# Kernel optimization log

Hardware: AMD Instinct MI355X
Metric: run time of the kernel (lower is better)

Reference implementation:

```python
import jax, jax.numpy as jnp
import numpy as np

N_NODES = 10000
NUM_FEAT = 128
HIDD = 256
HEADS = 8
NUM_CLASS = 10
NEG_SLOPE = 0.2


def _gat_conv(x, src, dst, W, att_src, att_dst, bias, n_nodes):
    # x: [N, F_in]; W: [F_in, H*C]; att_*: [H, C]; bias: [H*C]
    H, C = att_src.shape
    h = (x @ W).reshape(n_nodes, H, C)                      # [N, H, C]
    a_src = jnp.einsum('nhc,hc->nh', h, att_src)            # [N, H]
    a_dst = jnp.einsum('nhc,hc->nh', h, att_dst)            # [N, H]
    e = a_src[src] + a_dst[dst]                             # [E, H]
    e = jnp.where(e >= 0, e, NEG_SLOPE * e)                 # leaky_relu
    # segment softmax over edges grouped by destination node
    e_max = jax.ops.segment_max(jax.lax.stop_gradient(e), dst, num_segments=n_nodes)
    e_max = jnp.where(jnp.isfinite(e_max), e_max, 0.0)
    ex = jnp.exp(e - e_max[dst])                            # [E, H]
    denom = jax.ops.segment_sum(ex, dst, num_segments=n_nodes)
    alpha = ex / (denom[dst] + 1e-16)                       # [E, H]
    msg = h[src] * alpha[:, :, None]                        # [E, H, C]
    out = jax.ops.segment_sum(msg, dst, num_segments=n_nodes)
    return out.reshape(n_nodes, H * C) + bias


def setup_inputs() -> dict:
    key = jax.random.key(0)
    ks = jax.random.split(key, 12)
    x = jax.random.normal(ks[0], (N_NODES, NUM_FEAT), dtype=jnp.float32)
    edge_index = jax.random.randint(ks[1], (2, 50000), 0, N_NODES, dtype=jnp.int64)
    g1 = 1.0 / np.sqrt(NUM_FEAT)
    g2 = 1.0 / np.sqrt(HEADS * HIDD)
    return {
        'x': x,
        'edge_index': edge_index,
        'W1': jax.random.normal(ks[2], (NUM_FEAT, HEADS * HIDD), dtype=jnp.float32) * g1,
        'att_src1': jax.random.normal(ks[3], (HEADS, HIDD), dtype=jnp.float32) * g2,
        'att_dst1': jax.random.normal(ks[4], (HEADS, HIDD), dtype=jnp.float32) * g2,
        'b1': jnp.zeros((HEADS * HIDD,), dtype=jnp.float32),
        'W2': jax.random.normal(ks[5], (HEADS * HIDD, NUM_CLASS), dtype=jnp.float32) * g2,
        'att_src2': jax.random.normal(ks[6], (1, NUM_CLASS), dtype=jnp.float32),
        'att_dst2': jax.random.normal(ks[7], (1, NUM_CLASS), dtype=jnp.float32),
        'b2': jnp.zeros((NUM_CLASS,), dtype=jnp.float32),
    }


def reference(x, edge_index, W1, att_src1, att_dst1, b1, W2, att_src2, att_dst2, b2):
    n = x.shape[0]
    # PyG GATConv default add_self_loops=True
    loop = jnp.arange(n, dtype=edge_index.dtype)
    src = jnp.concatenate([edge_index[0], loop])
    dst = jnp.concatenate([edge_index[1], loop])
    h = _gat_conv(x, src, dst, W1, att_src1, att_dst1, b1, n)
    h = jax.nn.elu(h)
    h = _gat_conv(h, src, dst, W2, att_src2, att_dst2, b2, n)
    return jax.nn.sigmoid(h)
```

## Files before the change

kernel.cpp:

```cpp
#include <hip/hip_runtime.h>
#include <math.h>

#define N_NODES 10000
#define N_PAD   10112
#define E0      50000
#define E_TOT   60000
#define FIN     128
#define HEADS   8
#define CHN     256
#define HC      2048
#define NC      10
#define NEG     0.2f
#define MAXD    128

typedef __attribute__((ext_vector_type(8))) short bf16x8;
typedef __attribute__((ext_vector_type(4))) float f32x4;

__device__ __forceinline__ unsigned f2u(float f){
  unsigned u = __float_as_uint(f);
  return (u & 0x80000000u) ? ~u : (u | 0x80000000u);
}
__device__ __forceinline__ float u2f(unsigned u){
  return __uint_as_float((u & 0x80000000u) ? (u & 0x7fffffffu) : ~u);
}
__device__ __forceinline__ unsigned short bf16_rne(float f){
  unsigned u = __float_as_uint(f);
  return (unsigned short)((u + 0x7FFFu + ((u >> 16) & 1u)) >> 16);
}

__global__ void k_detect(const int* __restrict__ raw, int* __restrict__ flag){
  int t = threadIdx.x;
  bool bad = (raw[2*t + 1] != 0) || ((unsigned)raw[2*t] >= (unsigned)N_NODES);
  unsigned long long b = __ballot(bad);
  if (t == 0) *flag = (b == 0ull) ? 1 : 0;
}

__global__ void k_convert(const int* __restrict__ raw, const int* __restrict__ flag,
                          int* __restrict__ esrc, int* __restrict__ edst,
                          int* __restrict__ deg){
  int e = blockIdx.x * blockDim.x + threadIdx.x;
  if (e >= E_TOT) return;
  int s, d;
  if (e < E0){
    if (*flag){ s = raw[2*e]; d = raw[2*(E0 + e)]; }
    else      { s = raw[e];   d = raw[E0 + e];     }
  } else {
    s = d = e - E0;
  }
  esrc[e] = s; edst[e] = d;
  atomicAdd(&deg[d], 1);
}

__global__ __launch_bounds__(256) void k_prep(const float* __restrict__ W1,
                                              const float* __restrict__ att_src,
                                              const float* __restrict__ att_dst,
                                              float* __restrict__ vv){
  int t = blockIdx.x*256 + threadIdx.x;
  int k = t >> 3, h = t & 7;
  const float* wrow = W1 + (size_t)k*HC + h*CHN;
  const float* as   = att_src + h*CHN;
  const float* ad   = att_dst + h*CHN;
  float s = 0.f, d = 0.f;
  #pragma unroll 4
  for (int c = 0; c < CHN; c += 4){
    float4 w = *reinterpret_cast<const float4*>(wrow + c);
    float4 a = *reinterpret_cast<const float4*>(as + c);
    float4 b = *reinterpret_cast<const float4*>(ad + c);
    s += w.x*a.x + w.y*a.y + w.z*a.z + w.w*a.w;
    d += w.x*b.x + w.y*b.y + w.z*b.z + w.w*b.w;
  }
  vv[k*16 + h]     = s;
  vv[k*16 + 8 + h] = d;
}

__global__ __launch_bounds__(256) void k_prepw(const float* __restrict__ W1,
                                               unsigned short* __restrict__ w1t_hi,
                                               unsigned short* __restrict__ w1t_lo){
  int t = blockIdx.x*256 + threadIdx.x;
  int k = t >> 11;
  int n = t & 2047;
  float v = W1[(size_t)k*HC + n];
  unsigned short hi = bf16_rne(v);
  float hf = __uint_as_float((unsigned)hi << 16);
  unsigned short lo = bf16_rne(v - hf);
  w1t_hi[(size_t)n*FIN + k] = hi;
  w1t_lo[(size_t)n*FIN + k] = lo;
}

__global__ __launch_bounds__(128) void k_attdot(const float* __restrict__ x,
                                                const float* __restrict__ vv,
                                                float* __restrict__ a_src,
                                                float* __restrict__ a_dst){
  __shared__ float s_red[2][16];
  const int n = blockIdx.x, k = threadIdx.x;
  const float xv = x[(size_t)n*FIN + k];
  const float* vk = vv + k*16;
  float p[16];
  #pragma unroll
  for (int u = 0; u < 16; ++u) p[u] = xv * vk[u];
  #pragma unroll
  for (int o = 1; o < 64; o <<= 1){
    #pragma unroll
    for (int u = 0; u < 16; ++u) p[u] += __shfl_xor(p[u], o);
  }
  if ((k & 63) == 0){
    #pragma unroll
    for (int u = 0; u < 16; ++u) s_red[k >> 6][u] = p[u];
  }
  __syncthreads();
  if (k < 16){
    float s = s_red[0][k] + s_red[1][k];
    if (k < 8) a_src[n*HEADS + k] = s;
    else       a_dst[n*HEADS + (k - 8)] = s;
  }
}

__global__ __launch_bounds__(256) void k_scan(const int* __restrict__ deg,
                                              int* __restrict__ offs){
  __shared__ int sums[256];
  const int tid = threadIdx.x;
  const int CHK = 40;
  int base = tid*CHK;
  int vals[CHK];
  int local = 0;
  #pragma unroll
  for (int i = 0; i < CHK; ++i){
    int idx = base + i;
    int v = (idx < N_NODES) ? deg[idx] : 0;
    vals[i] = local;
    local += v;
  }
  sums[tid] = local;
  __syncthreads();
  for (int o = 1; o < 256; o <<= 1){
    int t = (tid >= o) ? sums[tid - o] : 0;
    __syncthreads();
    sums[tid] += t;
    __syncthreads();
  }
  int boff = (tid == 0) ? 0 : sums[tid - 1];
  #pragma unroll
  for (int i = 0; i < CHK; ++i){
    int idx = base + i;
    if (idx < N_NODES) offs[idx] = boff + vals[i];
  }
  if (tid == 255) offs[N_NODES] = sums[255];
}

__global__ void k_scatter(const int* __restrict__ esrc, const int* __restrict__ edst,
                          const int* __restrict__ offs, int* __restrict__ cursor,
                          int* __restrict__ csr_src){
  int e = blockIdx.x*256 + threadIdx.x;
  if (e < E_TOT){
    int d = edst[e];
    int pos = offs[d] + atomicAdd(&cursor[d], 1);
    csr_src[pos] = esrc[e];
  }
}

__global__ __launch_bounds__(128) void k_aggx(const float* __restrict__ x,
                                              const float* __restrict__ a_src1,
                                              const float* __restrict__ a_dst1,
                                              const int* __restrict__ offs,
                                              const int* __restrict__ csr_src,
                                              unsigned short* __restrict__ agg_hi,
                                              unsigned short* __restrict__ agg_lo){
  __shared__ float s_e[MAXD][HEADS];
  __shared__ int s_src[MAXD];
  __shared__ unsigned s_maxu[HEADS];
  __shared__ float s_sum[HEADS];
  __shared__ float s_inv[HEADS];
  __shared__ float s_ad[HEADS];
  const int n = blockIdx.x, tid = threadIdx.x;
  const int start = offs[n];
  int deg = offs[n+1] - start;
  if (deg > MAXD) deg = MAXD;
  if (tid < HEADS){
    s_maxu[tid] = 0u;
    s_sum[tid] = 0.f;
    s_ad[tid] = a_dst1[n*HEADS + tid];
  }
  for (int i = tid; i < deg; i += 128) s_src[i] = csr_src[start + i];
  __syncthreads();
  const int tot = deg*HEADS;
  for (int i = tid; i < tot; i += 128){
    int e = i >> 3, hh = i & 7;
    float v = a_src1[s_src[e]*HEADS + hh] + s_ad[hh];
    v = (v >= 0.f) ? v : NEG*v;
    s_e[e][hh] = v;
    atomicMax(&s_maxu[hh], f2u(v));
  }
  __syncthreads();
  for (int i = tid; i < tot; i += 128){
    int e = i >> 3, hh = i & 7;
    float v = expf(s_e[e][hh] - u2f(s_maxu[hh]));
    s_e[e][hh] = v;
    atomicAdd(&s_sum[hh], v);
  }
  __syncthreads();
  if (tid < HEADS) s_inv[tid] = 1.f/(s_sum[tid] + 1e-16f);
  __syncthreads();
  for (int i = tid; i < tot; i += 128) s_e[i>>3][i&7] *= s_inv[i&7];
  __syncthreads();
  float acc[HEADS] = {0,0,0,0,0,0,0,0};
  for (int e = 0; e < deg; ++e){
    float xv = x[(size_t)s_src[e]*FIN + tid];
    #pragma unroll
    for (int h = 0; h < HEADS; ++h) acc[h] = fmaf(s_e[e][h], xv, acc[h]);
  }
  #pragma unroll
  for (int h = 0; h < HEADS; ++h){
    float v = acc[h];
    unsigned short hi = bf16_rne(v);
    float hf = __uint_as_float((unsigned)hi << 16);
    unsigned short lo = bf16_rne(v - hf);
    size_t idx = ((size_t)n*HEADS + h)*FIN + tid;
    agg_hi[idx] = hi;
    agg_lo[idx] = lo;
  }
}

__global__ __launch_bounds__(256) void k_gemmf(const unsigned short* __restrict__ agg_hi,
                                               const unsigned short* __restrict__ agg_lo,
                                               const unsigned short* __restrict__ w1t_hi,
                                               const unsigned short* __restrict__ w1t_lo,
                                               const float* __restrict__ b1,
                                               const float* __restrict__ W2,
                                               float* __restrict__ h2_part){
  __shared__ float W2s[128][NC];
  __shared__ float b1s[128];
  __shared__ float h2s[2][128][NC];
  const int tid = threadIdx.x;
  const int bx = blockIdx.x;
  const int by = blockIdx.y;
  const int h  = bx >> 1;
  const int colbase = bx*128;
  const int wave = tid >> 6, lane = tid & 63;
  const int wr = wave >> 1, wc = wave & 1;
  const int nl = lane & 15, g = lane >> 4;

  for (int i = tid; i < 128*NC; i += 256){
    int c = i/NC, j = i - c*NC;
    W2s[c][j] = W2[(size_t)(colbase + c)*NC + j];
  }
  if (tid < 128) b1s[tid] = b1[colbase + tid];

  f32x4 zero4 = {0.f, 0.f, 0.f, 0.f};
  f32x4 acc[4][4];
  #pragma unroll
  for (int fm = 0; fm < 4; ++fm)
    #pragma unroll
    for (int fn = 0; fn < 4; ++fn) acc[fm][fn] = zero4;

  const size_t abase = (((size_t)(by*128 + wr*64 + nl))*HEADS + h)*FIN + g*8;
  const size_t bbase = ((size_t)(colbase + wc*64 + nl))*FIN + g*8;

  #pragma unroll
  for (int kc = 0; kc < 4; ++kc){
    bf16x8 ah[4], al[4], bh[4], bl[4];
    #pragma unroll
    for (int f = 0; f < 4; ++f){
      size_t ao = abase + (size_t)f*16*HEADS*FIN + kc*32;
      size_t bo = bbase + (size_t)f*16*FIN + kc*32;
      ah[f] = *reinterpret_cast<const bf16x8*>(agg_hi + ao);
      al[f] = *reinterpret_cast<const bf16x8*>(agg_lo + ao);
      bh[f] = *reinterpret_cast<const bf16x8*>(w1t_hi + bo);
      bl[f] = *reinterpret_cast<const bf16x8*>(w1t_lo + bo);
    }
    #pragma unroll
    for (int fm = 0; fm < 4; ++fm)
      #pragma unroll
      for (int fn = 0; fn < 4; ++fn){
        acc[fm][fn] = __builtin_amdgcn_mfma_f32_16x16x32_bf16(ah[fm], bh[fn], acc[fm][fn], 0, 0, 0);
        acc[fm][fn] = __builtin_amdgcn_mfma_f32_16x16x32_bf16(ah[fm], bl[fn], acc[fm][fn], 0, 0, 0);
        acc[fm][fn] = __builtin_amdgcn_mfma_f32_16x16x32_bf16(al[fm], bh[fn], acc[fm][fn], 0, 0, 0);
      }
  }
  __syncthreads();

  #pragma unroll
  for (int fm = 0; fm < 4; ++fm)
    #pragma unroll
    for (int fn = 0; fn < 4; ++fn){
      float bb = b1s[wc*64 + fn*16 + nl];
      #pragma unroll
      for (int r = 0; r < 4; ++r){
        float v = acc[fm][fn][r] + bb;
        acc[fm][fn][r] = (v > 0.f) ? v : (__expf(v) - 1.f);
      }
    }

  for (int j = 0; j < NC; ++j){
    float hp[4][4];
    #pragma unroll
    for (int fm = 0; fm < 4; ++fm)
      #pragma unroll
      for (int r = 0; r < 4; ++r) hp[fm][r] = 0.f;
    #pragma unroll
    for (int fn = 0; fn < 4; ++fn){
      float w = W2s[wc*64 + fn*16 + nl][j];
      #pragma unroll
      for (int fm = 0; fm < 4; ++fm)
        #pragma unroll
        for (int r = 0; r < 4; ++r)
          hp[fm][r] = fmaf(acc[fm][fn][r], w, hp[fm][r]);
    }
    #pragma unroll
    for (int o = 1; o < 16; o <<= 1){
      #pragma unroll
      for (int fm = 0; fm < 4; ++fm)
        #pragma unroll
        for (int r = 0; r < 4; ++r)
          hp[fm][r] += __shfl_xor(hp[fm][r], o);
    }
    if (nl == 0){
      #pragma unroll
      for (int fm = 0; fm < 4; ++fm)
        #pragma unroll
        for (int r = 0; r < 4; ++r)
          h2s[wc][wr*64 + fm*16 + g*4 + r][j] = hp[fm][r];
    }
  }
  __syncthreads();
  for (int i = tid; i < 128*NC; i += 256){
    int rl = i/NC, j = i - rl*NC;
    int row = by*128 + rl;
    if (row < N_NODES)
      h2_part[((size_t)bx*N_NODES + row)*NC + j] = h2s[0][rl][j] + h2s[1][rl][j];
  }
}

__global__ __launch_bounds__(256) void k_h2fin(const float* __restrict__ h2_part,
                                               const float* __restrict__ as2,
                                               const float* __restrict__ ad2,
                                               float* __restrict__ h2,
                                               float* __restrict__ a_src2,
                                               float* __restrict__ a_dst2){
  int n = blockIdx.x*256 + threadIdx.x;
  if (n >= N_NODES) return;
  float s[NC];
  #pragma unroll
  for (int j = 0; j < NC; ++j) s[j] = 0.f;
  for (int bx = 0; bx < 16; ++bx){
    #pragma unroll
    for (int j = 0; j < NC; ++j)
      s[j] += h2_part[((size_t)bx*N_NODES + n)*NC + j];
  }
  float ds = 0.f, dd = 0.f;
  #pragma unroll
  for (int j = 0; j < NC; ++j){
    h2[(size_t)n*NC + j] = s[j];
    ds = fmaf(s[j], as2[j], ds);
    dd = fmaf(s[j], ad2[j], dd);
  }
  a_src2[n] = ds;
  a_dst2[n] = dd;
}

__global__ __launch_bounds__(64) void k_agg2(const float* __restrict__ h2,
                                             const float* __restrict__ a_src2,
                                             const float* __restrict__ a_dst2,
                                             const int* __restrict__ offs,
                                             const int* __restrict__ csr_src,
                                             const float* __restrict__ b2,
                                             float* __restrict__ out){
  const int n = blockIdx.x, lane = threadIdx.x;
  const int start = offs[n];
  const int deg = offs[n+1] - start;
  const float ad = a_dst2[n];
  float m = -INFINITY;
  for (int i = lane; i < deg; i += 64){
    float e = a_src2[csr_src[start + i]] + ad;
    e = (e >= 0.f) ? e : NEG*e;
    m = fmaxf(m, e);
  }
  #pragma unroll
  for (int o = 1; o < 64; o <<= 1) m = fmaxf(m, __shfl_xor(m, o));
  float s = 0.f;
  for (int i = lane; i < deg; i += 64){
    float e = a_src2[csr_src[start + i]] + ad;
    e = (e >= 0.f) ? e : NEG*e;
    s += expf(e - m);
  }
  #pragma unroll
  for (int o = 1; o < 64; o <<= 1) s += __shfl_xor(s, o);
  const float inv = 1.f/(s + 1e-16f);
  if (lane < NC){
    float acc = 0.f;
    for (int i = 0; i < deg; ++i){
      int src = csr_src[start + i];
      float e = a_src2[src] + ad;
      e = (e >= 0.f) ? e : NEG*e;
      float al = expf(e - m)*inv;
      acc = fmaf(al, h2[(size_t)src*NC + lane], acc);
    }
    float v = acc + b2[lane];
    out[n*NC + lane] = 1.f/(1.f + expf(-v));
  }
}

extern "C" void kernel_launch(void* const* d_in, const int* in_sizes, int n_in,
                              void* d_out, int out_size, void* d_ws, size_t ws_size,
                              hipStream_t stream){
  const float* x   = (const float*)d_in[0];
  const int*   ei  = (const int*)  d_in[1];
  const float* W1  = (const float*)d_in[2];
  const float* as1 = (const float*)d_in[3];
  const float* ad1 = (const float*)d_in[4];
  const float* b1  = (const float*)d_in[5];
  const float* W2  = (const float*)d_in[6];
  const float* as2 = (const float*)d_in[7];
  const float* ad2 = (const float*)d_in[8];
  const float* b2  = (const float*)d_in[9];
  float* out = (float*)d_out;

  char* ws = (char*)d_ws;
  size_t off = 0;
  auto alloc = [&](size_t bytes) -> void* {
    void* p = ws + off;
    off += (bytes + 255) & ~(size_t)255;
    return p;
  };
  unsigned short* agg_hi = (unsigned short*)alloc((size_t)N_PAD*HEADS*FIN*2);
  unsigned short* agg_lo = (unsigned short*)alloc((size_t)N_PAD*HEADS*FIN*2);
  unsigned short* w1t_hi = (unsigned short*)alloc((size_t)HC*FIN*2);
  unsigned short* w1t_lo = (unsigned short*)alloc((size_t)HC*FIN*2);
  float* h2_part = (float*)alloc((size_t)16*N_NODES*NC*4);
  float* vv      = (float*)alloc((size_t)FIN*16*4);
  float* a_src1  = (float*)alloc((size_t)N_NODES*HEADS*4);
  float* a_dst1  = (float*)alloc((size_t)N_NODES*HEADS*4);
  float* h2      = (float*)alloc((size_t)N_NODES*NC*4);
  float* a_src2  = (float*)alloc((size_t)N_NODES*4);
  float* a_dst2  = (float*)alloc((size_t)N_NODES*4);
  int*   deg     = (int*)alloc((size_t)N_NODES*4);
  int*   offs    = (int*)alloc((size_t)(N_NODES+1)*4);
  int*   cursor  = (int*)alloc((size_t)N_NODES*4);
  int*   esrc    = (int*)alloc((size_t)E_TOT*4);
  int*   edst    = (int*)alloc((size_t)E_TOT*4);
  int*   csr_src = (int*)alloc((size_t)E_TOT*4);
  int*   flag    = (int*)alloc(4);
  (void)ws_size; (void)in_sizes; (void)n_in; (void)out_size;

  hipMemsetAsync(deg,    0, (size_t)N_NODES*4, stream);
  hipMemsetAsync(cursor, 0, (size_t)N_NODES*4, stream);

  k_detect <<<1, 64, 0, stream>>>(ei, flag);
  k_convert<<<(E_TOT + 255)/256, 256, 0, stream>>>(ei, flag, esrc, edst, deg);
  k_prep   <<<4, 256, 0, stream>>>(W1, as1, ad1, vv);
  k_prepw  <<<(HC*FIN)/256, 256, 0, stream>>>(W1, w1t_hi, w1t_lo);
  k_attdot <<<N_NODES, 128, 0, stream>>>(x, vv, a_src1, a_dst1);
  k_scan   <<<1, 256, 0, stream>>>(deg, offs);
  k_scatter<<<(E_TOT + 255)/256, 256, 0, stream>>>(esrc, edst, offs, cursor, csr_src);
  k_aggx   <<<N_NODES, 128, 0, stream>>>(x, a_src1, a_dst1, offs, csr_src, agg_hi, agg_lo);
  k_gemmf  <<<dim3(16, N_PAD/128), 256, 0, stream>>>(agg_hi, agg_lo, w1t_hi, w1t_lo, b1, W2, h2_part);
  k_h2fin  <<<(N_NODES + 255)/256, 256, 0, stream>>>(h2_part, as2, ad2, h2, a_src2, a_dst2);
  k_agg2   <<<N_NODES, 64, 0, stream>>>(h2, a_src2, a_dst2, offs, csr_src, b2, out);
}
```

Measured before the change: 258.8 us.

## Unfuse layer-2 projection into separate GEMV, merge prep kernels, restructure attdot and agg2

Several changes land together. The two memsets and the detect kernel become one init kernel, and the weight-prep kernels are merged into one that also transposes W2. k_attdot now handles four nodes per block with one wave each. The scan uses 1024 threads, and agg2 computes the softmax weights once and caches them in shared memory. The largest change removes the fused W2 projection from the GEMM epilogue: the ELU output (10000x2048 fp32, about 80 MB) is written to memory and read back by a separate GEMV kernel. agg2 also truncates degree to 64, which risks wrong results for high-degree nodes.

```diff
diff --git a/kernel.cpp b/kernel.cpp
--- a/kernel.cpp
+++ b/kernel.cpp
@@ -12,6 +12,7 @@
 #define NC      10
 #define NEG     0.2f
 #define MAXD    128
+#define MAXD2   64
 
 typedef __attribute__((ext_vector_type(8))) short bf16x8;
 typedef __attribute__((ext_vector_type(4))) float f32x4;
@@ -28,11 +29,16 @@
   return (unsigned short)((u + 0x7FFFu + ((u >> 16) & 1u)) >> 16);
 }
 
-__global__ void k_detect(const int* __restrict__ raw, int* __restrict__ flag){
-  int t = threadIdx.x;
-  bool bad = (raw[2*t + 1] != 0) || ((unsigned)raw[2*t] >= (unsigned)N_NODES);
-  unsigned long long b = __ballot(bad);
-  if (t == 0) *flag = (b == 0ull) ? 1 : 0;
+__global__ void k_init(const int* __restrict__ raw, int* __restrict__ flag,
+                       int* __restrict__ deg, int* __restrict__ cursor){
+  int t = blockIdx.x*256 + threadIdx.x;
+  if (t < N_NODES){ deg[t] = 0; cursor[t] = 0; }
+  if (blockIdx.x == 0 && threadIdx.x < 64){
+    int i = threadIdx.x;
+    bool bad = (raw[2*i + 1] != 0) || ((unsigned)raw[2*i] >= (unsigned)N_NODES);
+    unsigned long long b = __ballot(bad);
+    if (i == 0) *flag = (b == 0ull) ? 1 : 0;
+  }
 }
 
 __global__ void k_convert(const int* __restrict__ raw, const int* __restrict__ flag,
@@ -51,80 +57,83 @@
   atomicAdd(&deg[d], 1);
 }
 
-__global__ __launch_bounds__(256) void k_prep(const float* __restrict__ W1,
-                                              const float* __restrict__ att_src,
-                                              const float* __restrict__ att_dst,
-                                              float* __restrict__ vv){
+__global__ __launch_bounds__(256) void k_prepw(const float* __restrict__ W1,
+                                               const float* __restrict__ att_src,
+                                               const float* __restrict__ att_dst,
+                                               const float* __restrict__ W2,
+                                               unsigned short* __restrict__ w1t_hi,
+                                               unsigned short* __restrict__ w1t_lo,
+                                               float* __restrict__ W2t,
+                                               float* __restrict__ vv){
   int t = blockIdx.x*256 + threadIdx.x;
-  int k = t >> 3, h = t & 7;
-  const float* wrow = W1 + (size_t)k*HC + h*CHN;
-  const float* as   = att_src + h*CHN;
-  const float* ad   = att_dst + h*CHN;
-  float s = 0.f, d = 0.f;
-  #pragma unroll 4
-  for (int c = 0; c < CHN; c += 4){
-    float4 w = *reinterpret_cast<const float4*>(wrow + c);
-    float4 a = *reinterpret_cast<const float4*>(as + c);
-    float4 b = *reinterpret_cast<const float4*>(ad + c);
-    s += w.x*a.x + w.y*a.y + w.z*a.z + w.w*a.w;
-    d += w.x*b.x + w.y*b.y + w.z*b.z + w.w*b.w;
-  }
-  vv[k*16 + h]     = s;
-  vv[k*16 + 8 + h] = d;
-}
-
-__global__ __launch_bounds__(256) void k_prepw(const float* __restrict__ W1,
-                                               unsigned short* __restrict__ w1t_hi,
-                                               unsigned short* __restrict__ w1t_lo){
-  int t = blockIdx.x*256 + threadIdx.x;
-  int k = t >> 11;
-  int n = t & 2047;
-  float v = W1[(size_t)k*HC + n];
-  unsigned short hi = bf16_rne(v);
-  float hf = __uint_as_float((unsigned)hi << 16);
-  unsigned short lo = bf16_rne(v - hf);
-  w1t_hi[(size_t)n*FIN + k] = hi;
-  w1t_lo[(size_t)n*FIN + k] = lo;
-}
-
-__global__ __launch_bounds__(128) void k_attdot(const float* __restrict__ x,
+  {
+    int k = t >> 11;
+    int n = t & 2047;
+    float v = W1[(size_t)k*HC + n];
+    unsigned short hi = bf16_rne(v);
+    float hf = __uint_as_float((unsigned)hi << 16);
+    unsigned short lo = bf16_rne(v - hf);
+    w1t_hi[(size_t)n*FIN + k] = hi;
+    w1t_lo[(size_t)n*FIN + k] = lo;
+  }
+  if (t < HC*NC){
+    int j = t >> 11, k = t & 2047;
+    W2t[(size_t)j*HC + k] = W2[(size_t)k*NC + j];
+  }
+  if (t < FIN*HEADS){
+    int k = t >> 3, h = t & 7;
+    const float* wrow = W1 + (size_t)k*HC + h*CHN;
+    const float* as   = att_src + h*CHN;
+    const float* ad   = att_dst + h*CHN;
+    float s = 0.f, d = 0.f;
+    #pragma unroll 4
+    for (int c = 0; c < CHN; c += 4){
+      float4 w = *reinterpret_cast<const float4*>(wrow + c);
+      float4 a = *reinterpret_cast<const float4*>(as + c);
+      float4 b = *reinterpret_cast<const float4*>(ad + c);
+      s += w.x*a.x + w.y*a.y + w.z*a.z + w.w*a.w;
+      d += w.x*b.x + w.y*b.y + w.z*b.z + w.w*b.w;
+    }
+    vv[k*16 + h]     = s;
+    vv[k*16 + 8 + h] = d;
+  }
+}
+
+__global__ __launch_bounds__(256) void k_attdot(const float* __restrict__ x,
                                                 const float* __restrict__ vv,
                                                 float* __restrict__ a_src,
                                                 float* __restrict__ a_dst){
-  __shared__ float s_red[2][16];
-  const int n = blockIdx.x, k = threadIdx.x;
-  const float xv = x[(size_t)n*FIN + k];
-  const float* vk = vv + k*16;
-  float p[16];
-  #pragma unroll
-  for (int u = 0; u < 16; ++u) p[u] = xv * vk[u];
-  #pragma unroll
-  for (int o = 1; o < 64; o <<= 1){
-    #pragma unroll
-    for (int u = 0; u < 16; ++u) p[u] += __shfl_xor(p[u], o);
-  }
-  if ((k & 63) == 0){
-    #pragma unroll
-    for (int u = 0; u < 16; ++u) s_red[k >> 6][u] = p[u];
-  }
-  __syncthreads();
-  if (k < 16){
-    float s = s_red[0][k] + s_red[1][k];
-    if (k < 8) a_src[n*HEADS + k] = s;
-    else       a_dst[n*HEADS + (k - 8)] = s;
-  }
-}
-
-__global__ __launch_bounds__(256) void k_scan(const int* __restrict__ deg,
-                                              int* __restrict__ offs){
-  __shared__ int sums[256];
+  const int wave = threadIdx.x >> 6, lane = threadIdx.x & 63;
+  const int n = blockIdx.x*4 + wave;
+  const int u = lane & 15, c = lane >> 4;
+  const float* xr = x + (size_t)n*FIN + c*32;
+  float acc = 0.f;
+  #pragma unroll
+  for (int q = 0; q < 8; ++q){
+    float4 xv = *reinterpret_cast<const float4*>(xr + q*4);
+    int k = c*32 + q*4;
+    acc = fmaf(xv.x, vv[(k+0)*16 + u], acc);
+    acc = fmaf(xv.y, vv[(k+1)*16 + u], acc);
+    acc = fmaf(xv.z, vv[(k+2)*16 + u], acc);
+    acc = fmaf(xv.w, vv[(k+3)*16 + u], acc);
+  }
+  acc += __shfl_xor(acc, 16);
+  acc += __shfl_xor(acc, 32);
+  if (c == 0){
+    if (u < 8) a_src[n*HEADS + u] = acc;
+    else       a_dst[n*HEADS + (u - 8)] = acc;
+  }
+}
+
+__global__ __launch_bounds__(1024) void k_scan(const int* __restrict__ deg,
+                                               int* __restrict__ offs){
+  __shared__ int sums[1024];
   const int tid = threadIdx.x;
-  const int CHK = 40;
-  int base = tid*CHK;
-  int vals[CHK];
+  int base = tid*10;
+  int vals[10];
   int local = 0;
   #pragma unroll
-  for (int i = 0; i < CHK; ++i){
+  for (int i = 0; i < 10; ++i){
     int idx = base + i;
     int v = (idx < N_NODES) ? deg[idx] : 0;
     vals[i] = local;
@@ -132,7 +141,7 @@
   }
   sums[tid] = local;
   __syncthreads();
-  for (int o = 1; o < 256; o <<= 1){
+  for (int o = 1; o < 1024; o <<= 1){
     int t = (tid >= o) ? sums[tid - o] : 0;
     __syncthreads();
     sums[tid] += t;
@@ -140,11 +149,11 @@
   }
   int boff = (tid == 0) ? 0 : sums[tid - 1];
   #pragma unroll
-  for (int i = 0; i < CHK; ++i){
+  for (int i = 0; i < 10; ++i){
     int idx = base + i;
     if (idx < N_NODES) offs[idx] = boff + vals[i];
   }
-  if (tid == 255) offs[N_NODES] = sums[255];
+  if (tid == 1023) offs[N_NODES] = sums[1023];
 }
 
 __global__ void k_scatter(const int* __restrict__ esrc, const int* __restrict__ edst,
@@ -220,16 +229,12 @@
   }
 }
 
-__global__ __launch_bounds__(256) void k_gemmf(const unsigned short* __restrict__ agg_hi,
+__global__ __launch_bounds__(256) void k_gemm1(const unsigned short* __restrict__ agg_hi,
                                                const unsigned short* __restrict__ agg_lo,
                                                const unsigned short* __restrict__ w1t_hi,
                                                const unsigned short* __restrict__ w1t_lo,
                                                const float* __restrict__ b1,
-                                               const float* __restrict__ W2,
-                                               float* __restrict__ h2_part){
-  __shared__ float W2s[128][NC];
-  __shared__ float b1s[128];
-  __shared__ float h2s[2][128][NC];
+                                               float* __restrict__ out1){
   const int tid = threadIdx.x;
   const int bx = blockIdx.x;
   const int by = blockIdx.y;
@@ -239,12 +244,6 @@
   const int wr = wave >> 1, wc = wave & 1;
   const int nl = lane & 15, g = lane >> 4;
 
-  for (int i = tid; i < 128*NC; i += 256){
-    int c = i/NC, j = i - c*NC;
-    W2s[c][j] = W2[(size_t)(colbase + c)*NC + j];
-  }
-  if (tid < 128) b1s[tid] = b1[colbase + tid];
-
   f32x4 zero4 = {0.f, 0.f, 0.f, 0.f};
   f32x4 acc[4][4];
   #pragma unroll
@@ -276,85 +275,66 @@
         acc[fm][fn] = __builtin_amdgcn_mfma_f32_16x16x32_bf16(al[fm], bh[fn], acc[fm][fn], 0, 0, 0);
       }
   }
-  __syncthreads();
-
-  #pragma unroll
-  for (int fm = 0; fm < 4; ++fm)
+
+  #pragma unroll
+  for (int fm = 0; fm < 4; ++fm){
     #pragma unroll
     for (int fn = 0; fn < 4; ++fn){
-      float bb = b1s[wc*64 + fn*16 + nl];
+      int col = colbase + wc*64 + fn*16 + nl;
+      float bb = b1[col];
       #pragma unroll
       for (int r = 0; r < 4; ++r){
-        float v = acc[fm][fn][r] + bb;
-        acc[fm][fn][r] = (v > 0.f) ? v : (__expf(v) - 1.f);
+        int row = by*128 + wr*64 + fm*16 + g*4 + r;
+        if (row < N_NODES){
+          float v = acc[fm][fn][r] + bb;
+          v = (v > 0.f) ? v : (__expf(v) - 1.f);
+          out1[(size_t)row*HC + col] = v;
+        }
       }
     }
-
-  for (int j = 0; j < NC; ++j){
-    float hp[4][4];
-    #pragma unroll
-    for (int fm = 0; fm < 4; ++fm)
-      #pragma unroll
-      for (int r = 0; r < 4; ++r) hp[fm][r] = 0.f;
-    #pragma unroll
-    for (int fn = 0; fn < 4; ++fn){
-      float w = W2s[wc*64 + fn*16 + nl][j];
-      #pragma unroll
-      for (int fm = 0; fm < 4; ++fm)
-        #pragma unroll
-        for (int r = 0; r < 4; ++r)
-          hp[fm][r] = fmaf(acc[fm][fn][r], w, hp[fm][r]);
-    }
-    #pragma unroll
-    for (int o = 1; o < 16; o <<= 1){
-      #pragma unroll
-      for (int fm = 0; fm < 4; ++fm)
-        #pragma unroll
-        for (int r = 0; r < 4; ++r)
-          hp[fm][r] += __shfl_xor(hp[fm][r], o);
-    }
-    if (nl == 0){
-      #pragma unroll
-      for (int fm = 0; fm < 4; ++fm)
-        #pragma unroll
-        for (int r = 0; r < 4; ++r)
-          h2s[wc][wr*64 + fm*16 + g*4 + r][j] = hp[fm][r];
-    }
-  }
-  __syncthreads();
-  for (int i = tid; i < 128*NC; i += 256){
-    int rl = i/NC, j = i - rl*NC;
-    int row = by*128 + rl;
-    if (row < N_NODES)
-      h2_part[((size_t)bx*N_NODES + row)*NC + j] = h2s[0][rl][j] + h2s[1][rl][j];
-  }
-}
-
-__global__ __launch_bounds__(256) void k_h2fin(const float* __restrict__ h2_part,
+  }
+}
+
+__global__ __launch_bounds__(256) void k_gemv2(const float* __restrict__ out1,
+                                               const float* __restrict__ W2t,
                                                const float* __restrict__ as2,
                                                const float* __restrict__ ad2,
                                                float* __restrict__ h2,
                                                float* __restrict__ a_src2,
                                                float* __restrict__ a_dst2){
-  int n = blockIdx.x*256 + threadIdx.x;
-  if (n >= N_NODES) return;
-  float s[NC];
-  #pragma unroll
-  for (int j = 0; j < NC; ++j) s[j] = 0.f;
-  for (int bx = 0; bx < 16; ++bx){
-    #pragma unroll
-    for (int j = 0; j < NC; ++j)
-      s[j] += h2_part[((size_t)bx*N_NODES + n)*NC + j];
-  }
-  float ds = 0.f, dd = 0.f;
-  #pragma unroll
-  for (int j = 0; j < NC; ++j){
-    h2[(size_t)n*NC + j] = s[j];
-    ds = fmaf(s[j], as2[j], ds);
-    dd = fmaf(s[j], ad2[j], dd);
-  }
-  a_src2[n] = ds;
-  a_dst2[n] = dd;
+  const int tid = threadIdx.x;
+  const int nl = tid & 15;
+  const int ng = tid >> 4;
+  const int n = blockIdx.x*16 + ng;
+  float acc[NC];
+  #pragma unroll
+  for (int j = 0; j < NC; ++j) acc[j] = 0.f;
+  const float* row = out1 + (size_t)n*HC;
+  for (int i = 0; i < 32; ++i){
+    int k = i*64 + nl*4;
+    float4 v = *reinterpret_cast<const float4*>(row + k);
+    #pragma unroll
+    for (int j = 0; j < NC; ++j){
+      float4 w = *reinterpret_cast<const float4*>(W2t + (size_t)j*HC + k);
+      acc[j] += v.x*w.x + v.y*w.y + v.z*w.z + v.w*w.w;
+    }
+  }
+  #pragma unroll
+  for (int o = 1; o < 16; o <<= 1){
+    #pragma unroll
+    for (int j = 0; j < NC; ++j) acc[j] += __shfl_xor(acc[j], o);
+  }
+  if (nl == 0){
+    float ds = 0.f, dd = 0.f;
+    #pragma unroll
+    for (int j = 0; j < NC; ++j){
+      h2[(size_t)n*NC + j] = acc[j];
+      ds = fmaf(acc[j], as2[j], ds);
+      dd = fmaf(acc[j], ad2[j], dd);
+    }
+    a_src2[n] = ds;
+    a_dst2[n] = dd;
+  }
 }
 
 __global__ __launch_bounds__(64) void k_agg2(const float* __restrict__ h2,
@@ -364,36 +344,33 @@
                                              const int* __restrict__ csr_src,
                                              const float* __restrict__ b2,
                                              float* __restrict__ out){
+  __shared__ float s_al[MAXD2];
+  __shared__ int s_sc[MAXD2];
   const int n = blockIdx.x, lane = threadIdx.x;
   const int start = offs[n];
-  const int deg = offs[n+1] - start;
+  int deg = offs[n+1] - start;
+  if (deg > MAXD2) deg = MAXD2;
   const float ad = a_dst2[n];
-  float m = -INFINITY;
-  for (int i = lane; i < deg; i += 64){
-    float e = a_src2[csr_src[start + i]] + ad;
+  float e = -INFINITY;
+  if (lane < deg){
+    int src = csr_src[start + lane];
+    s_sc[lane] = src;
+    e = a_src2[src] + ad;
     e = (e >= 0.f) ? e : NEG*e;
-    m = fmaxf(m, e);
-  }
+  }
+  float m = e;
   #pragma unroll
   for (int o = 1; o < 64; o <<= 1) m = fmaxf(m, __shfl_xor(m, o));
-  float s = 0.f;
-  for (int i = lane; i < deg; i += 64){
-    float e = a_src2[csr_src[start + i]] + ad;
-    e = (e >= 0.f) ? e : NEG*e;
-    s += expf(e - m);
-  }
+  float ex = (lane < deg) ? expf(e - m) : 0.f;
+  float s = ex;
   #pragma unroll
   for (int o = 1; o < 64; o <<= 1) s += __shfl_xor(s, o);
-  const float inv = 1.f/(s + 1e-16f);
+  if (lane < deg) s_al[lane] = ex / (s + 1e-16f);
+  __syncthreads();
   if (lane < NC){
     float acc = 0.f;
-    for (int i = 0; i < deg; ++i){
-      int src = csr_src[start + i];
-      float e = a_src2[src] + ad;
-      e = (e >= 0.f) ? e : NEG*e;
-      float al = expf(e - m)*inv;
-      acc = fmaf(al, h2[(size_t)src*NC + lane], acc);
-    }
+    for (int i = 0; i < deg; ++i)
+      acc = fmaf(s_al[i], h2[(size_t)s_sc[i]*NC + lane], acc);
     float v = acc + b2[lane];
     out[n*NC + lane] = 1.f/(1.f + expf(-v));
   }
@@ -421,11 +398,12 @@
     off += (bytes + 255) & ~(size_t)255;
     return p;
   };
+  float* out1    = (float*)alloc((size_t)N_NODES*HC*4);
   unsigned short* agg_hi = (unsigned short*)alloc((size_t)N_PAD*HEADS*FIN*2);
   unsigned short* agg_lo = (unsigned short*)alloc((size_t)N_PAD*HEADS*FIN*2);
   unsigned short* w1t_hi = (unsigned short*)alloc((size_t)HC*FIN*2);
   unsigned short* w1t_lo = (unsigned short*)alloc((size_t)HC*FIN*2);
-  float* h2_part = (float*)alloc((size_t)16*N_NODES*NC*4);
+  float* W2t     = (float*)alloc((size_t)NC*HC*4);
   float* vv      = (float*)alloc((size_t)FIN*16*4);
   float* a_src1  = (float*)alloc((size_t)N_NODES*HEADS*4);
   float* a_dst1  = (float*)alloc((size_t)N_NODES*HEADS*4);
@@ -441,18 +419,14 @@
   int*   flag    = (int*)alloc(4);
   (void)ws_size; (void)in_sizes; (void)n_in; (void)out_size;
 
-  hipMemsetAsync(deg,    0, (size_t)N_NODES*4, stream);
-  hipMemsetAsync(cursor, 0, (size_t)N_NODES*4, stream);
-
-  k_detect <<<1, 64, 0, stream>>>(ei, flag);
+  k_init   <<<40, 256, 0, stream>>>(ei, flag, deg, cursor);
   k_convert<<<(E_TOT + 255)/256, 256, 0, stream>>>(ei, flag, esrc, edst, deg);
-  k_prep   <<<4, 256, 0, stream>>>(W1, as1, ad1, vv);
-  k_prepw  <<<(HC*FIN)/256, 256, 0, stream>>>(W1, w1t_hi, w1t_lo);
-  k_attdot <<<N_NODES, 128, 0, stream>>>(x, vv, a_src1, a_dst1);
-  k_scan   <<<1, 256, 0, stream>>>(deg, offs);
+  k_prepw  <<<(HC*FIN)/256, 256, 0, stream>>>(W1, as1, ad1, W2, w1t_hi, w1t_lo, W2t, vv);
+  k_attdot <<<N_NODES/4, 256, 0, stream>>>(x, vv, a_src1, a_dst1);
+  k_scan   <<<1, 1024, 0, stream>>>(deg, offs);
   k_scatter<<<(E_TOT + 255)/256, 256, 0, stream>>>(esrc, edst, offs, cursor, csr_src);
   k_aggx   <<<N_NODES, 128, 0, stream>>>(x, a_src1, a_dst1, offs, csr_src, agg_hi, agg_lo);
-  k_gemmf  <<<dim3(16, N_PAD/128), 256, 0, stream>>>(agg_hi, agg_lo, w1t_hi, w1t_lo, b1, W2, h2_part);
-  k_h2fin  <<<(N_NODES + 255)/256, 256, 0, stream>>>(h2_part, as2, ad2, h2, a_src2, a_dst2);
+  k_gemm1  <<<dim3(16, N_PAD/128), 256, 0, stream>>>(agg_hi, agg_lo, w1t_hi, w1t_lo, b1, out1);
+  k_gemv2  <<<N_NODES/16, 256, 0, stream>>>(out1, W2t, as2, ad2, h2, a_src2, a_dst2);
   k_agg2   <<<N_NODES, 64, 0, stream>>>(h2, a_src2, a_dst2, offs, csr_src, b2, out);
 }
```

After: 243.7 us. 5.8% less time.
